# Kernel optimization log

Measured on AMD Instinct MI355X. Metric: run time of the kernel, lower is better.

The kernel has to match this reference:

```python
import jax, jax.numpy as jnp
import numpy as np

N_ENT = 50000
N_REL = 500
IN_DIM = 128
OUT_DIM = 128
N_EDGES = 500000
LRELU_SLOPE = 0.01  # torch F.leaky_relu default


def setup_inputs() -> dict:
    key = jax.random.key(0)
    ks = jax.random.split(key, 8)
    # triplets [3, E]: row0=src entity, row1=relation, row2=dst entity.
    # Ensure every entity appears as a source so no 0/0 in the edge-softmax division.
    src_extra = jax.random.randint(ks[0], (N_EDGES - N_ENT,), 0, N_ENT)
    src = jnp.concatenate([jnp.arange(N_ENT), src_extra])
    rel = jax.random.randint(ks[1], (N_EDGES,), 0, N_REL)
    dst = jax.random.randint(ks[2], (N_EDGES,), 0, N_ENT)
    triplets = jnp.stack([src, rel, dst]).astype(jnp.int64)
    ent_embed = jax.random.normal(ks[3], (N_ENT, IN_DIM), dtype=jnp.float32)
    rel_embed = jax.random.normal(ks[4], (N_REL, IN_DIM), dtype=jnp.float32)
    adj = jax.random.randint(ks[5], (2, N_EDGES), 0, N_ENT).astype(jnp.int64)  # unused by forward
    # Xavier-normal (gain=1.414) init for the two linear layers, like the torch module.
    std_a = 1.414 * np.sqrt(2.0 / (3 * IN_DIM + OUT_DIM))
    std_a2 = 1.414 * np.sqrt(2.0 / (OUT_DIM + 1))
    W_a = jax.random.normal(ks[6], (3 * IN_DIM, OUT_DIM), dtype=jnp.float32) * std_a
    b_a = jnp.zeros((OUT_DIM,), dtype=jnp.float32)
    W_a2 = jax.random.normal(ks[7], (OUT_DIM, 1), dtype=jnp.float32) * std_a2
    b_a2 = jnp.zeros((1,), dtype=jnp.float32)
    return {"triplets": triplets, "ent_embed": ent_embed, "rel_embed": rel_embed,
            "adj": adj, "W_a": W_a, "b_a": b_a, "W_a2": W_a2, "b_a2": b_a2}


def reference(triplets, ent_embed, rel_embed, adj, W_a, b_a, W_a2, b_a2):
    src, rel, dst = triplets[0], triplets[1], triplets[2]
    n_ent = ent_embed.shape[0]
    # Gather + concat: [E, 3*in_dim]
    h = jnp.concatenate([ent_embed[src], rel_embed[rel], ent_embed[dst]], axis=1)
    c = h @ W_a + b_a                                   # [E, out_dim]
    b = jax.nn.leaky_relu(c @ W_a2 + b_a2, LRELU_SLOPE)  # [E, 1]
    e_b = jnp.exp(b)                                    # [E, 1]
    # Sparse edge-softmax grouped by source node (sparse.sum over dst dim).
    denom = jax.ops.segment_sum(e_b, src, num_segments=n_ent)        # [N, 1]
    numer = jax.ops.segment_sum(e_b * c, src, num_segments=n_ent)    # [N, out_dim]
    out = numer / denom
    return jax.nn.elu(out)  # concat=True branch
```

## Files before the change

### kernel.cpp

```cpp
#include <hip/hip_runtime.h>

#define DIM 128

typedef __attribute__((ext_vector_type(8))) short bf16x8;
typedef __attribute__((ext_vector_type(4))) float f32x4;

__device__ inline unsigned short to_bf16(float f) {
    unsigned u = __float_as_uint(f);
    u = (u + 0x7FFFu + ((u >> 16) & 1u)) >> 16;
    return (unsigned short)u;
}
__device__ inline unsigned pack_bf16(float lo, float hi) {
    return (unsigned)to_bf16(lo) | ((unsigned)to_bf16(hi) << 16);
}
__device__ inline float unpack_lo(unsigned v) { return __uint_as_float(v << 16); }
__device__ inline float unpack_hi(unsigned v) { return __uint_as_float(v & 0xFFFF0000u); }

__global__ void wprep_kernel(const float* __restrict__ W_a, unsigned short* __restrict__ Wt,
                             int* __restrict__ counts, int n) {
    const int c = blockIdx.x;
    const int k = threadIdx.x;
    const int srow = (c < 128) ? k : (256 + k);
    const int scol = (c < 128) ? c : (c - 128);
    Wt[c * DIM + k] = to_bf16(W_a[srow * DIM + scol]);
    for (int i = blockIdx.x * 128 + k; i < n; i += 256 * 128) counts[i] = 0;
}

__global__ __launch_bounds__(512, 4) void stage1_kernel(
        const float* __restrict__ ent, const float* __restrict__ rel,
        const int* __restrict__ T, const unsigned short* __restrict__ Wt,
        const float* __restrict__ W_rel, const float* __restrict__ b_a,
        const float* __restrict__ Wa2,
        unsigned* __restrict__ P1h, unsigned* __restrict__ P3h, unsigned* __restrict__ P2h,
        float* __restrict__ q1, float* __restrict__ q3, float* __restrict__ q2,
        int* __restrict__ counts, int NE, int NR, int E, int GB, int HB, int RB) {
    __shared__ unsigned smem[16640];
    int b = blockIdx.x;
    const int t = threadIdx.x;

    if (b < GB) {
        const int mrow = b * 128;
        const int wv = t >> 6;
        const int lane = t & 63;
        const int g = lane >> 4, m = lane & 15;

        #pragma unroll
        for (int i = 0; i < 8; ++i) {
            const int ci  = i * 8 + wv;
            const int row = ci * 4 + (lane >> 4);
            const int dw0 = (lane & 15) * 4;
            const int sdw = dw0 ^ ((row & 7) << 2);
            const uint4 v = *(const uint4*)(Wt + row * DIM + sdw * 2);
            *(uint4*)&smem[ci * 256 + lane * 4] = v;
        }

        const int rowA = min(mrow + wv * 16 + m, NE - 1);
        const float* arow = ent + (size_t)rowA * DIM;
        bf16x8 afrag[4];
        #pragma unroll
        for (int kk = 0; kk < 4; ++kk) {
            const float4 u0 = *(const float4*)(arow + kk * 32 + g * 8);
            const float4 u1 = *(const float4*)(arow + kk * 32 + g * 8 + 4);
            bf16x8 a;
            a[0] = (short)to_bf16(u0.x); a[1] = (short)to_bf16(u0.y);
            a[2] = (short)to_bf16(u0.z); a[3] = (short)to_bf16(u0.w);
            a[4] = (short)to_bf16(u1.x); a[5] = (short)to_bf16(u1.y);
            a[6] = (short)to_bf16(u1.z); a[7] = (short)to_bf16(u1.w);
            afrag[kk] = a;
        }
        __syncthreads();

        f32x4 acc[2][8];
        #pragma unroll
        for (int h = 0; h < 2; ++h)
            #pragma unroll
            for (int ct = 0; ct < 8; ++ct) acc[h][ct] = (f32x4){0.f, 0.f, 0.f, 0.f};
        #pragma unroll
        for (int kk = 0; kk < 4; ++kk) {
            #pragma unroll
            for (int h = 0; h < 2; ++h) {
                #pragma unroll
                for (int ct = 0; ct < 8; ++ct) {
                    const int brow = h * 128 + ct * 16 + m;
                    const int dw = (kk * 16 + g * 4) ^ ((brow & 7) << 2);
                    const bf16x8 bb = *(const bf16x8*)&smem[brow * 64 + dw];
                    acc[h][ct] = __builtin_amdgcn_mfma_f32_16x16x32_bf16(afrag[kk], bb, acc[h][ct], 0, 0, 0);
                }
            }
        }
        __syncthreads();

        unsigned short* lds16 = (unsigned short*)smem;
        #pragma unroll
        for (int h = 0; h < 2; ++h) {
            float* __restrict__ qo = h ? q3 : q1;
            float qp[4] = {0.f, 0.f, 0.f, 0.f};
            #pragma unroll
            for (int ct = 0; ct < 8; ++ct) {
                const int c = ct * 16 + m;
                const float bias = h ? 0.0f : b_a[c];
                const float wa2  = Wa2[c];
                #pragma unroll
                for (int r = 0; r < 4; ++r) {
                    const float v = acc[h][ct][r] + bias;
                    qp[r] += v * wa2;
                    lds16[(h * 128 + wv * 16 + g * 4 + r) * 130 + c] = to_bf16(v);
                }
            }
            #pragma unroll
            for (int r = 0; r < 4; ++r) {
                float v = qp[r];
                #pragma unroll
                for (int o = 1; o < 16; o <<= 1) v += __shfl_xor(v, o);
                const int row = mrow + wv * 16 + g * 4 + r;
                if (m == 0 && row < NE) qo[row] = v;
            }
        }
        __syncthreads();
        #pragma unroll 4
        for (int i = 0; i < 32; ++i) {
            const int linear = i * 512 + t;
            const int row = linear >> 6, d = linear & 63;
            const int rg = mrow + (row & 127);
            unsigned* __restrict__ Ph = (row < 128) ? P1h : P3h;
            if (rg < NE) Ph[(size_t)rg * 64 + d] = smem[row * 65 + d];
        }
        return;
    }
    b -= GB;

    if (b < HB) {
        for (int e = b * 512 + t; e < E; e += HB * 512)
            atomicAdd(&counts[T[e]], 1);
        return;
    }
    b -= HB;

    {
        float* xs   = (float*)smem;
        float* sred = (float*)(smem + 2048);
        const int row0 = b * 16;
        const int qr = t >> 7;
        const int tc = t & 127;
        #pragma unroll
        for (int e = 0; e < 4; ++e) {
            int row = row0 + qr * 4 + e;
            xs[(qr * 4 + e) * DIM + tc] = (row < NR) ? rel[(size_t)row * DIM + tc] : 0.0f;
        }
        __syncthreads();
        float acc[4] = {0.f, 0.f, 0.f, 0.f};
        #pragma unroll 4
        for (int k = 0; k < DIM; ++k) {
            const float wv = W_rel[k * DIM + tc];
            #pragma unroll
            for (int e = 0; e < 4; ++e) acc[e] += xs[(qr * 4 + e) * DIM + k] * wv;
        }
        const float wa2 = Wa2[tc];
        const int lane = t & 63;
        #pragma unroll
        for (int e = 0; e < 4; ++e) {
            float v = acc[e] * wa2;
            #pragma unroll
            for (int o = 32; o > 0; o >>= 1) v += __shfl_down(v, o);
            if (lane == 0) sred[(qr * 4 + e) * 2 + ((t >> 6) & 1)] = v;
        }
        __syncthreads();
        #pragma unroll
        for (int e = 0; e < 4; ++e) {
            int row = row0 + qr * 4 + e;
            float hi = __shfl_down(acc[e], 1);
            if (row < NR && (tc & 1) == 0)
                P2h[(size_t)row * 64 + (tc >> 1)] = pack_bf16(acc[e], hi);
        }
        if (t < 16) {
            int row = row0 + t;
            if (row < NR) q2[row] = sred[t * 2] + sred[t * 2 + 1];
        }
    }
}

__device__ inline int wave_incl_scan(int v) {
    const int lane = threadIdx.x & 63;
    #pragma unroll
    for (int o = 1; o < 64; o <<= 1) {
        int u = __shfl_up(v, o);
        if (lane >= o) v += u;
    }
    return v;
}

__global__ __launch_bounds__(256) void scan_bsum_kernel(const int* __restrict__ counts,
                                                        int* __restrict__ bsum, int n) {
    __shared__ int ws[4];
    const int t = threadIdx.x;
    const int base = blockIdx.x * 1024 + t * 4;
    int s = 0;
    #pragma unroll
    for (int j = 0; j < 4; ++j) if (base + j < n) s += counts[base + j];
    #pragma unroll
    for (int o = 32; o > 0; o >>= 1) s += __shfl_down(s, o);
    if ((t & 63) == 0) ws[t >> 6] = s;
    __syncthreads();
    if (t == 0) bsum[blockIdx.x] = ws[0] + ws[1] + ws[2] + ws[3];
}

__global__ __launch_bounds__(256) void scan_write_kernel(const int* __restrict__ counts,
        const int* __restrict__ bsum, int* __restrict__ offsets, int* __restrict__ cursor,
        int n, int total, int nb) {
    __shared__ int s_boff, wsum[4], wpre[4];
    const int t = threadIdx.x;
    if (t < 64) {
        int v = (t < nb) ? bsum[t] : 0;
        int incl = wave_incl_scan(v);
        int ex = incl - v;
        int want = __shfl(ex, (int)blockIdx.x);
        if (t == 0) s_boff = want;
    }
    const int base = blockIdx.x * 1024 + t * 4;
    int c[4];
    int s = 0;
    #pragma unroll
    for (int j = 0; j < 4; ++j) {
        c[j] = (base + j < n) ? counts[base + j] : 0;
        s += c[j];
    }
    int incl = wave_incl_scan(s);
    const int wid = t >> 6, lane = t & 63;
    if (lane == 63) wsum[wid] = incl;
    __syncthreads();
    if (t == 0) {
        int run = 0;
        #pragma unroll
        for (int k = 0; k < 4; ++k) { wpre[k] = run; run += wsum[k]; }
    }
    __syncthreads();
    int run = incl - s + wpre[wid] + s_boff;
    #pragma unroll
    for (int j = 0; j < 4; ++j) {
        if (base + j < n) { offsets[base + j] = run; cursor[base + j] = run; run += c[j]; }
    }
    if (base == 0 && blockIdx.x == 0) offsets[n] = total;
}

__global__ void scatter_kernel(const int* __restrict__ T, const float* __restrict__ q1,
                               const float* __restrict__ q2, const float* __restrict__ q3,
                               const float* __restrict__ b_a2, int* __restrict__ cursor,
                               uint2* __restrict__ rdw, int E) {
    const int e = blockIdx.x * blockDim.x + threadIdx.x;
    if (e >= E) return;
    const int s = T[e], r = T[E + e], d = T[2 * E + e];
    float b = q1[s] + q2[r] + q3[d] + b_a2[0];
    b = (b > 0.0f) ? b : 0.01f * b;
    const float wv = __expf(b);
    const int pos = atomicAdd(&cursor[s], 1);
    rdw[pos] = make_uint2(((unsigned)r << 17) | (unsigned)d, __float_as_uint(wv));
}

__global__ void gather_kernel(const int* __restrict__ offsets, const uint2* __restrict__ rdw,
                              const unsigned* __restrict__ P1h, const unsigned* __restrict__ P2h,
                              const unsigned* __restrict__ P3h, float* __restrict__ out, int n) {
    const int node = (blockIdx.x << 2) + (threadIdx.x >> 6);
    if (node >= n) return;
    const int lane = threadIdx.x & 63;
    const int lo = offsets[node], hi = offsets[node + 1];
    const unsigned p1 = P1h[(size_t)node * 64 + lane];
    float axp[4] = {0.f,0.f,0.f,0.f};
    float ayp[4] = {0.f,0.f,0.f,0.f};
    float wsp[4] = {0.f,0.f,0.f,0.f};
    for (int i = lo; i < hi; i += 8) {
        uint2 e[8];
        float wgt[8];
        #pragma unroll
        for (int j = 0; j < 8; ++j) {
            const int idx = min(i + j, hi - 1);
            e[j] = rdw[idx];
            wgt[j] = (i + j < hi) ? __uint_as_float(e[j].y) : 0.0f;
        }
        unsigned v2[8], v3[8];
        #pragma unroll
        for (int j = 0; j < 8; ++j) {
            v2[j] = P2h[(size_t)(e[j].x >> 17) * 64 + lane];
            v3[j] = P3h[(size_t)(e[j].x & 0x1FFFFu) * 64 + lane];
        }
        #pragma unroll
        for (int j = 0; j < 8; ++j) {
            axp[j & 3] += wgt[j] * (unpack_lo(v2[j]) + unpack_lo(v3[j]));
            ayp[j & 3] += wgt[j] * (unpack_hi(v2[j]) + unpack_hi(v3[j]));
            wsp[j & 3] += wgt[j];
        }
    }
    const float ax = (axp[0] + axp[1]) + (axp[2] + axp[3]);
    const float ay = (ayp[0] + ayp[1]) + (ayp[2] + ayp[3]);
    const float inv = 1.0f / ((wsp[0] + wsp[1]) + (wsp[2] + wsp[3]));
    float v0 = unpack_lo(p1) + ax * inv;
    float v1 = unpack_hi(p1) + ay * inv;
    v0 = (v0 > 0.0f) ? v0 : (__expf(v0) - 1.0f);
    v1 = (v1 > 0.0f) ? v1 : (__expf(v1) - 1.0f);
    *(float2*)(out + (size_t)node * DIM + (lane << 1)) = make_float2(v0, v1);
}

extern "C" void kernel_launch(void* const* d_in, const int* in_sizes, int n_in,
                              void* d_out, int out_size, void* d_ws, size_t ws_size,
                              hipStream_t stream) {
    const int*   T    = (const int*)d_in[0];
    const float* ent  = (const float*)d_in[1];
    const float* rel  = (const float*)d_in[2];
    const float* W_a  = (const float*)d_in[4];
    const float* b_a  = (const float*)d_in[5];
    const float* W_a2 = (const float*)d_in[6];
    const float* b_a2 = (const float*)d_in[7];
    float* out = (float*)d_out;

    const int E  = in_sizes[0] / 3;
    const int NE = in_sizes[1] / DIM;
    const int NR = in_sizes[2] / DIM;
    const int NB = (NE + 1023) / 1024;
    const int GB = (NE + 127) / 128;
    const int HB = 128;
    const int RB = (NR + 15) / 16;

    float* ws = (float*)d_ws;
    size_t off = 0;
    unsigned* P1h = (unsigned*)(ws + off); off += (size_t)NE * 64;
    unsigned* P3h = (unsigned*)(ws + off); off += (size_t)NE * 64;
    unsigned* P2h = (unsigned*)(ws + off); off += (size_t)NR * 64;
    unsigned short* Wt = (unsigned short*)(ws + off); off += 256 * DIM / 2;
    float* q1   = ws + off; off += NE;
    float* q3   = ws + off; off += NE;
    float* q2   = ws + off; off += NR + 64;
    int* counts  = (int*)(ws + off); off += NE;
    int* offsets = (int*)(ws + off); off += NE + 64;
    int* cursor  = (int*)(ws + off); off += NE;
    int* bsum    = (int*)(ws + off); off += 64;
    uint2* rdw   = (uint2*)(ws + off); off += (size_t)E * 2;

    wprep_kernel<<<256, 128, 0, stream>>>(W_a, Wt, counts, NE);

    stage1_kernel<<<GB + HB + RB, 512, 0, stream>>>(
        ent, rel, T, Wt, W_a + 128 * DIM, b_a, W_a2,
        P1h, P3h, P2h, q1, q3, q2, counts, NE, NR, E, GB, HB, RB);

    scan_bsum_kernel<<<NB, 256, 0, stream>>>(counts, bsum, NE);
    scan_write_kernel<<<NB, 256, 0, stream>>>(counts, bsum, offsets, cursor, NE, E, NB);

    scatter_kernel<<<(E + 255) / 256, 256, 0, stream>>>(T, q1, q2, q3, b_a2, cursor, rdw, E);

    gather_kernel<<<(NE + 3) / 4, 256, 0, stream>>>(offsets, rdw, P1h, P2h, P3h, out, NE);
}
```

Baseline: 98.51 us.

## Fuse two-pass scan via decoupled lookback; vectorize histogram and scatter edges

Replaces the two scan kernels with one kernel in which each block publishes its partial sum to a state array and spins until all block sums are visible, which removes one kernel launch. The histogram and scatter paths now read four source/relation/destination indices at a time with int4 loads, so fewer threads issue wider reads. The spin-wait only works if all 49 scan blocks are resident at the same time, which holds for this grid size. The scatter grid also becomes smaller.

```diff
diff --git a/kernel.cpp b/kernel.cpp
--- a/kernel.cpp
+++ b/kernel.cpp
@@ -17,13 +17,14 @@
 __device__ inline float unpack_hi(unsigned v) { return __uint_as_float(v & 0xFFFF0000u); }
 
 __global__ void wprep_kernel(const float* __restrict__ W_a, unsigned short* __restrict__ Wt,
-                             int* __restrict__ counts, int n) {
+                             int* __restrict__ counts, int* __restrict__ state, int n) {
     const int c = blockIdx.x;
     const int k = threadIdx.x;
     const int srow = (c < 128) ? k : (256 + k);
     const int scol = (c < 128) ? c : (c - 128);
     Wt[c * DIM + k] = to_bf16(W_a[srow * DIM + scol]);
     for (int i = blockIdx.x * 128 + k; i < n; i += 256 * 128) counts[i] = 0;
+    if (c == 0 && k < 64) state[k] = 0;
 }
 
 __global__ __launch_bounds__(512, 4) void stage1_kernel(
@@ -130,8 +131,15 @@
     b -= GB;
 
     if (b < HB) {
-        for (int e = b * 512 + t; e < E; e += HB * 512)
-            atomicAdd(&counts[T[e]], 1);
+        const int E4 = E >> 2;
+        for (int i = b * 512 + t; i < E4; i += HB * 512) {
+            const int4 s4 = *(const int4*)(T + i * 4);
+            atomicAdd(&counts[s4.x], 1);
+            atomicAdd(&counts[s4.y], 1);
+            atomicAdd(&counts[s4.z], 1);
+            atomicAdd(&counts[s4.w], 1);
+        }
+        if (b == 0 && t < (E & 3)) atomicAdd(&counts[T[(E & ~3) + t]], 1);
         return;
     }
     b -= HB;
@@ -189,34 +197,15 @@
     return v;
 }
 
-__global__ __launch_bounds__(256) void scan_bsum_kernel(const int* __restrict__ counts,
-                                                        int* __restrict__ bsum, int n) {
-    __shared__ int ws[4];
+__global__ __launch_bounds__(256) void scan_fused_kernel(
+        const int* __restrict__ counts, int* __restrict__ state,
+        int* __restrict__ offsets, int* __restrict__ cursor,
+        int n, int total, int nb) {
+    __shared__ int wsum[4], wpre[4];
+    __shared__ int s_boff;
+    const int b = blockIdx.x;
     const int t = threadIdx.x;
-    const int base = blockIdx.x * 1024 + t * 4;
-    int s = 0;
-    #pragma unroll
-    for (int j = 0; j < 4; ++j) if (base + j < n) s += counts[base + j];
-    #pragma unroll
-    for (int o = 32; o > 0; o >>= 1) s += __shfl_down(s, o);
-    if ((t & 63) == 0) ws[t >> 6] = s;
-    __syncthreads();
-    if (t == 0) bsum[blockIdx.x] = ws[0] + ws[1] + ws[2] + ws[3];
-}
-
-__global__ __launch_bounds__(256) void scan_write_kernel(const int* __restrict__ counts,
-        const int* __restrict__ bsum, int* __restrict__ offsets, int* __restrict__ cursor,
-        int n, int total, int nb) {
-    __shared__ int s_boff, wsum[4], wpre[4];
-    const int t = threadIdx.x;
-    if (t < 64) {
-        int v = (t < nb) ? bsum[t] : 0;
-        int incl = wave_incl_scan(v);
-        int ex = incl - v;
-        int want = __shfl(ex, (int)blockIdx.x);
-        if (t == 0) s_boff = want;
-    }
-    const int base = blockIdx.x * 1024 + t * 4;
+    const int base = b * 1024 + t * 4;
     int c[4];
     int s = 0;
     #pragma unroll
@@ -232,6 +221,16 @@
         int run = 0;
         #pragma unroll
         for (int k = 0; k < 4; ++k) { wpre[k] = run; run += wsum[k]; }
+        atomicExch(&state[b], run + 1);
+    }
+    if (t < 64) {
+        int v = 0;
+        if (t < nb) {
+            do { v = atomicAdd(&state[t], 0); } while (v == 0);
+            v -= 1;
+        }
+        int vincl = wave_incl_scan(v);
+        if (t == b) s_boff = vincl - v;
     }
     __syncthreads();
     int run = incl - s + wpre[wid] + s_boff;
@@ -239,21 +238,41 @@
     for (int j = 0; j < 4; ++j) {
         if (base + j < n) { offsets[base + j] = run; cursor[base + j] = run; run += c[j]; }
     }
-    if (base == 0 && blockIdx.x == 0) offsets[n] = total;
+    if (base == 0 && b == 0) offsets[n] = total;
 }
 
 __global__ void scatter_kernel(const int* __restrict__ T, const float* __restrict__ q1,
                                const float* __restrict__ q2, const float* __restrict__ q3,
                                const float* __restrict__ b_a2, int* __restrict__ cursor,
                                uint2* __restrict__ rdw, int E) {
-    const int e = blockIdx.x * blockDim.x + threadIdx.x;
-    if (e >= E) return;
-    const int s = T[e], r = T[E + e], d = T[2 * E + e];
-    float b = q1[s] + q2[r] + q3[d] + b_a2[0];
-    b = (b > 0.0f) ? b : 0.01f * b;
-    const float wv = __expf(b);
-    const int pos = atomicAdd(&cursor[s], 1);
-    rdw[pos] = make_uint2(((unsigned)r << 17) | (unsigned)d, __float_as_uint(wv));
+    const int i = blockIdx.x * blockDim.x + threadIdx.x;
+    const int E4 = E >> 2;
+    const float qc = b_a2[0];
+    if (i < E4) {
+        const int4 s4 = *(const int4*)(T + i * 4);
+        const int4 r4 = *(const int4*)(T + E + i * 4);
+        const int4 d4 = *(const int4*)(T + 2 * E + i * 4);
+        const int ss[4] = {s4.x, s4.y, s4.z, s4.w};
+        const int rr[4] = {r4.x, r4.y, r4.z, r4.w};
+        const int dd[4] = {d4.x, d4.y, d4.z, d4.w};
+        #pragma unroll
+        for (int j = 0; j < 4; ++j) {
+            float bb = q1[ss[j]] + q2[rr[j]] + q3[dd[j]] + qc;
+            bb = (bb > 0.0f) ? bb : 0.01f * bb;
+            const float wv = __expf(bb);
+            const int pos = atomicAdd(&cursor[ss[j]], 1);
+            rdw[pos] = make_uint2(((unsigned)rr[j] << 17) | (unsigned)dd[j], __float_as_uint(wv));
+        }
+    } else if (i == E4 && (E & 3)) {
+        for (int e = E & ~3; e < E; ++e) {
+            const int s = T[e], r = T[E + e], d = T[2 * E + e];
+            float bb = q1[s] + q2[r] + q3[d] + qc;
+            bb = (bb > 0.0f) ? bb : 0.01f * bb;
+            const float wv = __expf(bb);
+            const int pos = atomicAdd(&cursor[s], 1);
+            rdw[pos] = make_uint2(((unsigned)r << 17) | (unsigned)d, __float_as_uint(wv));
+        }
+    }
 }
 
 __global__ void gather_kernel(const int* __restrict__ offsets, const uint2* __restrict__ rdw,
@@ -331,19 +350,18 @@
     int* counts  = (int*)(ws + off); off += NE;
     int* offsets = (int*)(ws + off); off += NE + 64;
     int* cursor  = (int*)(ws + off); off += NE;
-    int* bsum    = (int*)(ws + off); off += 64;
+    int* state   = (int*)(ws + off); off += 64;
     uint2* rdw   = (uint2*)(ws + off); off += (size_t)E * 2;
 
-    wprep_kernel<<<256, 128, 0, stream>>>(W_a, Wt, counts, NE);
+    wprep_kernel<<<256, 128, 0, stream>>>(W_a, Wt, counts, state, NE);
 
     stage1_kernel<<<GB + HB + RB, 512, 0, stream>>>(
         ent, rel, T, Wt, W_a + 128 * DIM, b_a, W_a2,
         P1h, P3h, P2h, q1, q3, q2, counts, NE, NR, E, GB, HB, RB);
 
-    scan_bsum_kernel<<<NB, 256, 0, stream>>>(counts, bsum, NE);
-    scan_write_kernel<<<NB, 256, 0, stream>>>(counts, bsum, offsets, cursor, NE, E, NB);
-
-    scatter_kernel<<<(E + 255) / 256, 256, 0, stream>>>(T, q1, q2, q3, b_a2, cursor, rdw, E);
+    scan_fused_kernel<<<NB, 256, 0, stream>>>(counts, state, offsets, cursor, NE, E, NB);
+
+    scatter_kernel<<<((E >> 2) + 256) / 256, 256, 0, stream>>>(T, q1, q2, q3, b_a2, cursor, rdw, E);
 
     gather_kernel<<<(NE + 3) / 4, 256, 0, stream>>>(offsets, rdw, P1h, P2h, P3h, out, NE);
 }
```

Result: no change. 98.66 us (+0.1%).
